# Performance work log

Measured on AMD Instinct MI355X. Metric: run time of the kernel, lower is better.

## Reference

```python
import jax, jax.numpy as jnp
import numpy as np

HIDDEN = 32
INPUT = 1


def setup_inputs() -> dict:
    key = jax.random.key(0)
    ks = jax.random.split(key, 8)
    B, T = 4096, 512
    s = 1.0 / np.sqrt(HIDDEN)
    return {
        "x": jax.random.normal(ks[0], (B, T, INPUT), dtype=jnp.float32),
        "h0": jnp.zeros((1, B, HIDDEN), dtype=jnp.float32),
        "W_ih": jax.random.uniform(ks[1], (HIDDEN, INPUT), jnp.float32, -s, s),
        "b_ih": jax.random.uniform(ks[2], (HIDDEN,), jnp.float32, -s, s),
        "W_hh": jax.random.uniform(ks[3], (HIDDEN, HIDDEN), jnp.float32, -s, s),
        "b_hh": jax.random.uniform(ks[4], (HIDDEN,), jnp.float32, -s, s),
        "W_out": jax.random.uniform(ks[5], (1, HIDDEN), jnp.float32, -s, s),
        "b_out": jax.random.uniform(ks[6], (1,), jnp.float32, -s, s),
    }


def reference(x, h0, W_ih, b_ih, W_hh, b_hh, W_out, b_out):
    # Precompute input projection for all timesteps: [B, T, H]
    xp = jnp.einsum("bti,hi->bth", x, W_ih) + b_ih

    def step(h, xt):  # h: [B,H], xt: [B,H]
        h_new = jnp.tanh(xt + h @ W_hh.T + b_hh)
        return h_new, h_new

    hT, r_out = jax.lax.scan(step, h0[0], jnp.swapaxes(xp, 0, 1))  # r_out: [T,B,H]
    r_out = jnp.swapaxes(r_out, 0, 1)  # [B,T,H]
    # Per-timestep Linear(32->1) fused into one batched matmul
    outs = jnp.einsum("bth,oh->bto", r_out, W_out) + b_out  # [B,T,1]
    return outs, hT[None]  # h_state: [1,B,H]
```

## Files before the change

### kernel.cpp

```cpp
#include <hip/hip_runtime.h>

#define BATCH 4096
#define SEQT  512
#define HID   32
#define CH    32
#define RSTRIDE 20
#define SEQSTRIDE (CH * RSTRIDE + 4)

typedef _Float16 f16;
typedef _Float16 h2 __attribute__((ext_vector_type(2)));

#if __has_builtin(__builtin_amdgcn_fdot2)
#define FDOT2(a, b, c) __builtin_amdgcn_fdot2((a), (b), (c), false)
#else
#define FDOT2(a, b, c) fmaf((float)(a)[1], (float)(b)[1], fmaf((float)(a)[0], (float)(b)[0], (c)))
#endif

#if __has_builtin(__builtin_amdgcn_exp2f)
#define FAST_EXP2(x) __builtin_amdgcn_exp2f(x)
#else
#define FAST_EXP2(x) exp2f(x)
#endif
#if __has_builtin(__builtin_amdgcn_rcpf)
#define FAST_RCP(x) __builtin_amdgcn_rcpf(x)
#else
#define FAST_RCP(x) (1.0f / (x))
#endif

#if __has_builtin(__builtin_amdgcn_update_dpp)
#define ROT16(v, i) __builtin_amdgcn_update_dpp(0, (v), 0x120 + (i), 0xF, 0xF, true)
#else
#define ROT16(v, i) __shfl((v), (int)((threadIdx.x & ~15u) | ((threadIdx.x + (i)) & 15u)), 64)
#endif

#define GATHER15(dst, src) \
    dst[1]  = ROT16(src, 1);  dst[2]  = ROT16(src, 2);  dst[3]  = ROT16(src, 3);  \
    dst[4]  = ROT16(src, 4);  dst[5]  = ROT16(src, 5);  dst[6]  = ROT16(src, 6);  \
    dst[7]  = ROT16(src, 7);  dst[8]  = ROT16(src, 8);  dst[9]  = ROT16(src, 9);  \
    dst[10] = ROT16(src, 10); dst[11] = ROT16(src, 11); dst[12] = ROT16(src, 12); \
    dst[13] = ROT16(src, 13); dst[14] = ROT16(src, 14); dst[15] = ROT16(src, 15);

#define BCI(x) __builtin_bit_cast(h2, (x))
#define BCF(x) __builtin_bit_cast(h2, (x))

static __device__ __forceinline__ int packh(float a, float b) {
    h2 v = {(f16)a, (f16)b};
    return __builtin_bit_cast(int, v);
}

__global__ __launch_bounds__(64) void rnn_kernel(
    const float* __restrict__ x,
    const float* __restrict__ h0,
    const float* __restrict__ W_ih,
    const float* __restrict__ b_ih,
    const float* __restrict__ W_hh,
    const float* __restrict__ b_hh,
    const float* __restrict__ W_out,
    const float* __restrict__ b_out,
    float* __restrict__ out)
{
    const int lane = threadIdx.x & 63;
    const int row  = lane >> 4;
    const int l    = lane & 15;
    const int bs0  = blockIdx.x * 4;
    const int bseq = bs0 + row;

    __shared__ __align__(16) float hist[4 * SEQSTRIDE];
    __shared__ float xbuf[4 * CH];

    int idx[16];
    idx[0] = l;
    GATHER15(idx, l);

    h2 Wr0[16], Wr1[16];
    #pragma unroll
    for (int i = 0; i < 16; ++i) {
        const int s = idx[i];
        Wr0[i] = h2{(f16)W_hh[l * HID + s],        (f16)W_hh[l * HID + s + 16]};
        Wr1[i] = h2{(f16)W_hh[(l + 16) * HID + s], (f16)W_hh[(l + 16) * HID + s + 16]};
    }
    h2 Wo[16];
    #pragma unroll
    for (int i = 0; i < 16; ++i)
        Wo[i] = h2{(f16)W_out[i], (f16)W_out[i + 16]};

    const float wih0  = W_ih[l];
    const float wih1  = W_ih[l + 16];
    const float bias0 = b_ih[l] + b_hh[l];
    const float bias1 = b_ih[l + 16] + b_hh[l + 16];
    const float bout  = b_out[0];

    int d0 = packh(h0[(size_t)bseq * HID + l], h0[(size_t)bseq * HID + l + 16]);

    const float* xg = x + (size_t)bs0 * SEQT;
    float*       og = out + (size_t)bs0 * SEQT;

    for (int tc = 0; tc < SEQT; tc += CH) {
        xbuf[lane]      = xg[(size_t)(lane >> 5) * SEQT + tc + (lane & 31)];
        xbuf[lane + 64] = xg[(size_t)((lane >> 5) + 2) * SEQT + tc + (lane & 31)];
        __builtin_amdgcn_wave_barrier();

        float xc = xbuf[row * CH];

        #pragma unroll 8
        for (int t2 = 0; t2 < CH; ++t2) {
            int d[16];
            d[0] = d0;
            GATHER15(d, d0);

            const float xn = xbuf[row * CH + ((t2 + 1) & (CH - 1))];

            float a00 = fmaf(xc, wih0, bias0);
            float a01 = 0.0f, a02 = 0.0f, a03 = 0.0f;
            float a10 = fmaf(xc, wih1, bias1);
            float a11 = 0.0f, a12 = 0.0f, a13 = 0.0f;
            #pragma unroll
            for (int i = 0; i < 4; ++i) {
                a00 = FDOT2(BCI(d[4 * i + 0]), Wr0[4 * i + 0], a00);
                a10 = FDOT2(BCI(d[4 * i + 0]), Wr1[4 * i + 0], a10);
                a01 = FDOT2(BCI(d[4 * i + 1]), Wr0[4 * i + 1], a01);
                a11 = FDOT2(BCI(d[4 * i + 1]), Wr1[4 * i + 1], a11);
                a02 = FDOT2(BCI(d[4 * i + 2]), Wr0[4 * i + 2], a02);
                a12 = FDOT2(BCI(d[4 * i + 2]), Wr1[4 * i + 2], a12);
                a03 = FDOT2(BCI(d[4 * i + 3]), Wr0[4 * i + 3], a03);
                a13 = FDOT2(BCI(d[4 * i + 3]), Wr1[4 * i + 3], a13);
            }
            const float p0 = (a00 + a01) + (a02 + a03);
            const float p1 = (a10 + a11) + (a12 + a13);

            const float e0  = FAST_EXP2(p0 * 2.8853900817779268f);
            const float e1  = FAST_EXP2(p1 * 2.8853900817779268f);
            const float hn0 = fmaf(-2.0f, FAST_RCP(e0 + 1.0f), 1.0f);
            const float hn1 = fmaf(-2.0f, FAST_RCP(e1 + 1.0f), 1.0f);

            d0 = packh(hn0, hn1);

            hist[row * SEQSTRIDE + t2 * RSTRIDE + l] = __builtin_bit_cast(float, d0);
            __builtin_amdgcn_wave_barrier();

            xc = xn;
        }

        #pragma unroll
        for (int c = 0; c < 2; ++c) {
            const int io  = lane + 64 * c;
            const int seq = io >> 5;
            const int t   = io & 31;
            const float4* hp =
                reinterpret_cast<const float4*>(&hist[seq * SEQSTRIDE + t * RSTRIDE]);
            const float4 q0 = hp[0], q1 = hp[1], q2 = hp[2], q3 = hp[3];
            float o0 = FDOT2(BCF(q0.x), Wo[0],  bout);
            float o1 = FDOT2(BCF(q0.y), Wo[1],  0.0f);
            float o2 = FDOT2(BCF(q0.z), Wo[2],  0.0f);
            float o3 = FDOT2(BCF(q0.w), Wo[3],  0.0f);
            o0 = FDOT2(BCF(q1.x), Wo[4],  o0);
            o1 = FDOT2(BCF(q1.y), Wo[5],  o1);
            o2 = FDOT2(BCF(q1.z), Wo[6],  o2);
            o3 = FDOT2(BCF(q1.w), Wo[7],  o3);
            o0 = FDOT2(BCF(q2.x), Wo[8],  o0);
            o1 = FDOT2(BCF(q2.y), Wo[9],  o1);
            o2 = FDOT2(BCF(q2.z), Wo[10], o2);
            o3 = FDOT2(BCF(q2.w), Wo[11], o3);
            o0 = FDOT2(BCF(q3.x), Wo[12], o0);
            o1 = FDOT2(BCF(q3.y), Wo[13], o1);
            o2 = FDOT2(BCF(q3.z), Wo[14], o2);
            o3 = FDOT2(BCF(q3.w), Wo[15], o3);
            og[(size_t)seq * SEQT + tc + t] = (o0 + o1) + (o2 + o3);
        }
        __builtin_amdgcn_wave_barrier();
    }

    const h2 hf = BCI(d0);
    out[(size_t)BATCH * SEQT + (size_t)bseq * HID + l]      = (float)hf[0];
    out[(size_t)BATCH * SEQT + (size_t)bseq * HID + l + 16] = (float)hf[1];
}

extern "C" void kernel_launch(void* const* d_in, const int* in_sizes, int n_in,
                              void* d_out, int out_size, void* d_ws, size_t ws_size,
                              hipStream_t stream) {
    const float* x     = (const float*)d_in[0];
    const float* h0    = (const float*)d_in[1];
    const float* W_ih  = (const float*)d_in[2];
    const float* b_ih  = (const float*)d_in[3];
    const float* W_hh  = (const float*)d_in[4];
    const float* b_hh  = (const float*)d_in[5];
    const float* W_out = (const float*)d_in[6];
    const float* b_out = (const float*)d_in[7];
    float* outp = (float*)d_out;

    dim3 grid(BATCH / 4);
    dim3 block(64);
    hipLaunchKernelGGL(rnn_kernel, grid, block, 0, stream,
                       x, h0, W_ih, b_ih, W_hh, b_hh, W_out, b_out, outp);
}
```

Measured before the change: 158.0 us.

## Map one hidden unit per lane, two sequences per wave, with xor-swizzle exchange

Each lane now computes a single hidden unit (32 lanes per sequence, two sequences per wave) instead of two units across 16 lanes for four sequences. The latency of the serial recurrence step is split over twice as many lanes, and the grid doubles to 2048 waves. The cost is an extra ds_swizzle xor exchange per step to rebuild the packed half2 state. The tanh scale is folded into the weights and bias, x is read straight from global as float4 prefetches instead of being staged in LDS, packing uses cvt_pkrtz, and the chunk shrinks to 16 steps. Round-toward-zero packing and pre-scaled fp16 weights slightly change numerics.

```diff
diff --git a/kernel.cpp b/kernel.cpp
--- a/kernel.cpp
+++ b/kernel.cpp
@@ -3,9 +3,9 @@
 #define BATCH 4096
 #define SEQT  512
 #define HID   32
-#define CH    32
-#define RSTRIDE 20
-#define SEQSTRIDE (CH * RSTRIDE + 4)
+#define CH    16
+#define RS    20
+#define SEQSTR (CH * RS + 16)
 
 typedef _Float16 f16;
 typedef _Float16 h2 __attribute__((ext_vector_type(2)));
@@ -40,12 +40,22 @@
     dst[10] = ROT16(src, 10); dst[11] = ROT16(src, 11); dst[12] = ROT16(src, 12); \
     dst[13] = ROT16(src, 13); dst[14] = ROT16(src, 14); dst[15] = ROT16(src, 15);
 
+#if __has_builtin(__builtin_amdgcn_ds_swizzle)
+#define XOR16(v) __builtin_amdgcn_ds_swizzle((v), 0x401F)
+#else
+#define XOR16(v) __shfl_xor((v), 16, 64)
+#endif
+
 #define BCI(x) __builtin_bit_cast(h2, (x))
 #define BCF(x) __builtin_bit_cast(h2, (x))
 
 static __device__ __forceinline__ int packh(float a, float b) {
+#if __has_builtin(__builtin_amdgcn_cvt_pkrtz)
+    return __builtin_bit_cast(int, __builtin_amdgcn_cvt_pkrtz(a, b));
+#else
     h2 v = {(f16)a, (f16)b};
     return __builtin_bit_cast(int, v);
+#endif
 }
 
 __global__ __launch_bounds__(64) void rnn_kernel(
@@ -60,94 +70,95 @@
     float* __restrict__ out)
 {
     const int lane = threadIdx.x & 63;
-    const int row  = lane >> 4;
+    const int g    = lane >> 5;
+    const int j    = lane & 31;
     const int l    = lane & 15;
-    const int bs0  = blockIdx.x * 4;
-    const int bseq = bs0 + row;
-
-    __shared__ __align__(16) float hist[4 * SEQSTRIDE];
-    __shared__ float xbuf[4 * CH];
+    const bool up  = (j & 16) != 0;
+    const int bs0  = blockIdx.x * 2;
+    const int bseq = bs0 + g;
+
+    __shared__ __align__(16) float hist[2 * SEQSTR];
 
     int idx[16];
     idx[0] = l;
     GATHER15(idx, l);
 
-    h2 Wr0[16], Wr1[16];
+    const float SC = 2.8853900817779268f;
+
+    h2 Wr[16];
     #pragma unroll
     for (int i = 0; i < 16; ++i) {
         const int s = idx[i];
-        Wr0[i] = h2{(f16)W_hh[l * HID + s],        (f16)W_hh[l * HID + s + 16]};
-        Wr1[i] = h2{(f16)W_hh[(l + 16) * HID + s], (f16)W_hh[(l + 16) * HID + s + 16]};
+        Wr[i] = h2{(f16)(W_hh[j * HID + s] * SC), (f16)(W_hh[j * HID + s + 16] * SC)};
     }
     h2 Wo[16];
     #pragma unroll
     for (int i = 0; i < 16; ++i)
         Wo[i] = h2{(f16)W_out[i], (f16)W_out[i + 16]};
 
-    const float wih0  = W_ih[l];
-    const float wih1  = W_ih[l + 16];
-    const float bias0 = b_ih[l] + b_hh[l];
-    const float bias1 = b_ih[l + 16] + b_hh[l + 16];
-    const float bout  = b_out[0];
+    const float wih  = W_ih[j] * SC;
+    const float bias = (b_ih[j] + b_hh[j]) * SC;
+    const float bout = b_out[0];
 
     int d0 = packh(h0[(size_t)bseq * HID + l], h0[(size_t)bseq * HID + l + 16]);
 
-    const float* xg = x + (size_t)bs0 * SEQT;
+    const float* xg = x + (size_t)bseq * SEQT;
     float*       og = out + (size_t)bs0 * SEQT;
 
+    float4 xq = *reinterpret_cast<const float4*>(xg);
+
+#define STEP(XC, T2)                                                          \
+    {                                                                         \
+        int d[16];                                                            \
+        d[0] = d0;                                                            \
+        GATHER15(d, d0);                                                      \
+        float a0 = fmaf((XC), wih, bias);                                     \
+        float a1 = FDOT2(BCI(d[1]), Wr[1], 0.0f);                             \
+        float a2 = FDOT2(BCI(d[2]), Wr[2], 0.0f);                             \
+        float a3 = FDOT2(BCI(d[3]), Wr[3], 0.0f);                             \
+        a0 = FDOT2(BCI(d[0]),  Wr[0],  a0);                                   \
+        a0 = FDOT2(BCI(d[4]),  Wr[4],  a0);                                   \
+        a1 = FDOT2(BCI(d[5]),  Wr[5],  a1);                                   \
+        a2 = FDOT2(BCI(d[6]),  Wr[6],  a2);                                   \
+        a3 = FDOT2(BCI(d[7]),  Wr[7],  a3);                                   \
+        a0 = FDOT2(BCI(d[8]),  Wr[8],  a0);                                   \
+        a1 = FDOT2(BCI(d[9]),  Wr[9],  a1);                                   \
+        a2 = FDOT2(BCI(d[10]), Wr[10], a2);                                   \
+        a3 = FDOT2(BCI(d[11]), Wr[11], a3);                                   \
+        a0 = FDOT2(BCI(d[12]), Wr[12], a0);                                   \
+        a1 = FDOT2(BCI(d[13]), Wr[13], a1);                                   \
+        a2 = FDOT2(BCI(d[14]), Wr[14], a2);                                   \
+        a3 = FDOT2(BCI(d[15]), Wr[15], a3);                                   \
+        const float p  = (a0 + a1) + (a2 + a3);         \
+        const float e  = FAST_EXP2(p);                                        \
+        const float hn = fmaf(-2.0f, FAST_RCP(e + 1.0f), 1.0f);               \
+        const float sw = __builtin_bit_cast(float,                            \
+                             XOR16(__builtin_bit_cast(int, hn)));             \
+        const float lo = up ? sw : hn;                           \
+        const float hi = up ? hn : sw;                           \
+        d0 = packh(lo, hi);                                                   \
+        hist[g * SEQSTR + (T2) * RS + l] = __builtin_bit_cast(float, d0);     \
+        __builtin_amdgcn_wave_barrier();                                      \
+    }
+
     for (int tc = 0; tc < SEQT; tc += CH) {
-        xbuf[lane]      = xg[(size_t)(lane >> 5) * SEQT + tc + (lane & 31)];
-        xbuf[lane + 64] = xg[(size_t)((lane >> 5) + 2) * SEQT + tc + (lane & 31)];
-        __builtin_amdgcn_wave_barrier();
-
-        float xc = xbuf[row * CH];
-
-        #pragma unroll 8
-        for (int t2 = 0; t2 < CH; ++t2) {
-            int d[16];
-            d[0] = d0;
-            GATHER15(d, d0);
-
-            const float xn = xbuf[row * CH + ((t2 + 1) & (CH - 1))];
-
-            float a00 = fmaf(xc, wih0, bias0);
-            float a01 = 0.0f, a02 = 0.0f, a03 = 0.0f;
-            float a10 = fmaf(xc, wih1, bias1);
-            float a11 = 0.0f, a12 = 0.0f, a13 = 0.0f;
-            #pragma unroll
-            for (int i = 0; i < 4; ++i) {
-                a00 = FDOT2(BCI(d[4 * i + 0]), Wr0[4 * i + 0], a00);
-                a10 = FDOT2(BCI(d[4 * i + 0]), Wr1[4 * i + 0], a10);
-                a01 = FDOT2(BCI(d[4 * i + 1]), Wr0[4 * i + 1], a01);
-                a11 = FDOT2(BCI(d[4 * i + 1]), Wr1[4 * i + 1], a11);
-                a02 = FDOT2(BCI(d[4 * i + 2]), Wr0[4 * i + 2], a02);
-                a12 = FDOT2(BCI(d[4 * i + 2]), Wr1[4 * i + 2], a12);
-                a03 = FDOT2(BCI(d[4 * i + 3]), Wr0[4 * i + 3], a03);
-                a13 = FDOT2(BCI(d[4 * i + 3]), Wr1[4 * i + 3], a13);
-            }
-            const float p0 = (a00 + a01) + (a02 + a03);
-            const float p1 = (a10 + a11) + (a12 + a13);
-
-            const float e0  = FAST_EXP2(p0 * 2.8853900817779268f);
-            const float e1  = FAST_EXP2(p1 * 2.8853900817779268f);
-            const float hn0 = fmaf(-2.0f, FAST_RCP(e0 + 1.0f), 1.0f);
-            const float hn1 = fmaf(-2.0f, FAST_RCP(e1 + 1.0f), 1.0f);
-
-            d0 = packh(hn0, hn1);
-
-            hist[row * SEQSTRIDE + t2 * RSTRIDE + l] = __builtin_bit_cast(float, d0);
-            __builtin_amdgcn_wave_barrier();
-
-            xc = xn;
+        #pragma unroll
+        for (int tg = 0; tg < CH; tg += 4) {
+            int tnext = tc + tg + 4;
+            if (tnext > SEQT - 4) tnext = SEQT - 4;
+            const float4 xqn = *reinterpret_cast<const float4*>(xg + tnext);
+            STEP(xq.x, tg + 0)
+            STEP(xq.y, tg + 1)
+            STEP(xq.z, tg + 2)
+            STEP(xq.w, tg + 3)
+            xq = xqn;
         }
 
-        #pragma unroll
-        for (int c = 0; c < 2; ++c) {
-            const int io  = lane + 64 * c;
-            const int seq = io >> 5;
-            const int t   = io & 31;
+        if (lane < 32) {
+            const int g2 = lane >> 4;
+            const int t  = lane & 15;
             const float4* hp =
-                reinterpret_cast<const float4*>(&hist[seq * SEQSTRIDE + t * RSTRIDE]);
+                reinterpret_cast<const float4*>(&hist[g2 * SEQSTR + t * RS]);
             const float4 q0 = hp[0], q1 = hp[1], q2 = hp[2], q3 = hp[3];
             float o0 = FDOT2(BCF(q0.x), Wo[0],  bout);
             float o1 = FDOT2(BCF(q0.y), Wo[1],  0.0f);
@@ -165,14 +176,14 @@
             o1 = FDOT2(BCF(q3.y), Wo[13], o1);
             o2 = FDOT2(BCF(q3.z), Wo[14], o2);
             o3 = FDOT2(BCF(q3.w), Wo[15], o3);
-            og[(size_t)seq * SEQT + tc + t] = (o0 + o1) + (o2 + o3);
+            og[(size_t)g2 * SEQT + tc + t] = (o0 + o1) + (o2 + o3);
         }
         __builtin_amdgcn_wave_barrier();
     }
+#undef STEP
 
     const h2 hf = BCI(d0);
-    out[(size_t)BATCH * SEQT + (size_t)bseq * HID + l]      = (float)hf[0];
-    out[(size_t)BATCH * SEQT + (size_t)bseq * HID + l + 16] = (float)hf[1];
+    out[(size_t)BATCH * SEQT + (size_t)bseq * HID + j] = up ? (float)hf[1] : (float)hf[0];
 }
 
 extern "C" void kernel_launch(void* const* d_in, const int* in_sizes, int n_in,
@@ -188,7 +199,7 @@
     const float* b_out = (const float*)d_in[7];
     float* outp = (float*)d_out;
 
-    dim3 grid(BATCH / 4);
+    dim3 grid(BATCH / 2);
     dim3 block(64);
     hipLaunchKernelGGL(rnn_kernel, grid, block, 0, stream,
                        x, h0, W_ih, b_ih, W_hh, b_hh, W_out, b_out, outp);
```

New measurement: 184.5 us. +16.8%, slower.
